# Performance work log

Measured on AMD Instinct MI355X. Metric: run time of the kernel, lower is better.

## Reference

```python
import jax, jax.numpy as jnp
import numpy as np

B, T, V, E, H, C = 64, 512, 50257, 128, 64, 20

def _lstm_params(key, in_dim, scale=0.05):
    k1, k2, k3 = jax.random.split(key, 3)
    return (jax.random.normal(k1, (in_dim, 4 * H)) * scale,
            jax.random.normal(k2, (H, 4 * H)) * scale,
            jax.random.normal(k3, (4 * H,)) * scale)

def setup_inputs():
    key = jax.random.key(0)
    ks = jax.random.split(key, 10)
    lengths = jax.random.randint(ks[0], (B,), T // 4, T + 1)
    mask = (jnp.arange(T)[None, :] < lengths[:, None]).astype(jnp.int32)
    ids = jax.random.randint(ks[1], (B, T), 1, V) * mask  # pad id 0 past length
    positions = jnp.broadcast_to(jnp.arange(T, dtype=jnp.int32), (B, T))
    x = jnp.stack([ids, positions, mask], axis=1)  # [B,3,T]
    inp = {"x": x,
           "word_emb": jax.random.normal(ks[2], (V, E)) * 0.05,
           "pos_emb": jax.random.normal(ks[3], (V, E)) * 0.05}
    for name, in_dim, kk in [("f0", E, ks[4]), ("f1", H, ks[5]), ("b0", E, ks[6]), ("b1", H, ks[7])]:
        Wx, Wh, b = _lstm_params(kk, in_dim)
        inp["wx_" + name] = Wx
        inp["wh_" + name] = Wh
        inp["b_" + name] = b
    inp["dense_w"] = jax.random.normal(ks[8], (H, C)) * 0.05
    inp["dense_b"] = jnp.zeros((C,), jnp.float32)
    return inp

def _lstm_layer(xs, mask, Wx, Wh, b, backwards):
    # xs: [B,T,D], mask: [B,T] bool. Keras masking semantics: at masked steps
    # hidden/cell state (and emitted output) carry over from the previous step.
    # go_backwards reverses inputs AND mask, and does NOT re-reverse outputs
    # (that is the raw keras LSTM behaviour without the Bidirectional wrapper).
    if backwards:
        xs = xs[:, ::-1]
        mask = mask[:, ::-1]
    xT = jnp.swapaxes(xs, 0, 1)    # [T,B,D]
    mT = jnp.swapaxes(mask, 0, 1)  # [T,B]
    h0 = jnp.zeros((xs.shape[0], H), xs.dtype)
    c0 = h0
    def step(carry, inp):
        h, c = carry
        x_t, m_t = inp
        z = x_t @ Wx + h @ Wh + b  # [B,4H], keras gate order i,f,g,o
        i = jax.nn.sigmoid(z[:, :H])
        f = jax.nn.sigmoid(z[:, H:2 * H])
        g = jnp.tanh(z[:, 2 * H:3 * H])
        o = jax.nn.sigmoid(z[:, 3 * H:])
        c_new = f * c + i * g
        h_new = o * jnp.tanh(c_new)
        m = m_t[:, None]
        h2 = jnp.where(m, h_new, h)
        c2 = jnp.where(m, c_new, c)
        return (h2, c2), h2
    _, hs = jax.lax.scan(step, (h0, c0), (xT, mT))
    return jnp.swapaxes(hs, 0, 1)  # [B,T,H]

def reference(x, word_emb, pos_emb, wx_f0, wh_f0, b_f0, wx_f1, wh_f1, b_f1,
              wx_b0, wh_b0, b_b0, wx_b1, wh_b1, b_b1, dense_w, dense_b):
    ids, positions, attn = x[:, 0, :], x[:, 1, :], x[:, 2, :]
    mask = attn.astype(bool)
    emb = word_emb[ids] + pos_emb[positions]  # [B,T,E]
    f = _lstm_layer(emb, mask, wx_f0, wh_f0, b_f0, False)
    f = _lstm_layer(f, mask, wx_f1, wh_f1, b_f1, False)
    bo = _lstm_layer(emb, mask, wx_b0, wh_b0, b_b0, True)
    bo = _lstm_layer(bo, mask, wx_b1, wh_b1, b_b1, True)
    # Concatenate(axis=1) stacks [fwd_out, bwd_out] along TIME, dense+softmax
    # per step, then [:, -1, :] -> only the last step of the backward stack
    # reaches the output (faithful to the original module).
    last = bo[:, -1, :]
    return jax.nn.softmax(last @ dense_w + dense_b, axis=-1)  # [B,C]
```

## Files before the change

### kernel.cpp

```cpp
#include <hip/hip_runtime.h>
#include <hip/hip_bf16.h>

#define Bn 64
#define Tn 512
#define En 128
#define Hn 64
#define Gn 256
#define Cn 20

__device__ __forceinline__ float sigf(float x)      { return 1.f/(1.f+__expf(-x)); }
__device__ __forceinline__ float tanhfast(float x)  { return 2.f/(1.f+__expf(-2.f*x)) - 1.f; }

__global__ __launch_bounds__(256, 1) void emb_proj_kernel(
    const int* __restrict__ x, const float* __restrict__ word_emb,
    const float* __restrict__ pos_emb, const float* __restrict__ wx,
    const float* __restrict__ bias, float* __restrict__ z0)
{
  __shared__ float emb[64][En];
  __shared__ float wxl[32][Gn];
  const int tid  = threadIdx.x;
  const int row0 = blockIdx.x * 64;

  #pragma unroll
  for (int it = 0; it < 8; ++it) {
    int idx = it*256 + tid;
    int rr  = idx >> 5;
    int e4  = (idx & 31) << 2;
    int r   = row0 + rr;
    int b   = r >> 9;
    int t   = r & (Tn-1);
    int id  = x[b*3*Tn + t];
    float4 we = *reinterpret_cast<const float4*>(&word_emb[(size_t)id*En + e4]);
    float4 pe = *reinterpret_cast<const float4*>(&pos_emb[(size_t)t*En + e4]);
    *reinterpret_cast<float4*>(&emb[rr][e4]) =
        make_float4(we.x+pe.x, we.y+pe.y, we.z+pe.z, we.w+pe.w);
  }

  const int jc = tid & 63;
  const int rg = tid >> 6;
  float acc[16][4];
  float4 bb = *reinterpret_cast<const float4*>(&bias[jc*4]);
  #pragma unroll
  for (int r = 0; r < 16; ++r) { acc[r][0]=bb.x; acc[r][1]=bb.y; acc[r][2]=bb.z; acc[r][3]=bb.w; }

  for (int ec = 0; ec < 4; ++ec) {
    __syncthreads();
    #pragma unroll
    for (int it = 0; it < 8; ++it) {
      int idx = it*256 + tid;
      int ee  = idx >> 6;
      int j4  = (idx & 63) << 2;
      *reinterpret_cast<float4*>(&wxl[ee][j4]) =
          *reinterpret_cast<const float4*>(&wx[(size_t)(ec*32+ee)*Gn + j4]);
    }
    __syncthreads();
    for (int ee = 0; ee < 32; ++ee) {
      float4 w = *reinterpret_cast<const float4*>(&wxl[ee][jc*4]);
      #pragma unroll
      for (int r = 0; r < 16; ++r) {
        float xv = emb[rg*16+r][ec*32+ee];
        acc[r][0] = fmaf(xv, w.x, acc[r][0]);
        acc[r][1] = fmaf(xv, w.y, acc[r][1]);
        acc[r][2] = fmaf(xv, w.z, acc[r][2]);
        acc[r][3] = fmaf(xv, w.w, acc[r][3]);
      }
    }
  }
  #pragma unroll
  for (int r = 0; r < 16; ++r) {
    size_t row = (size_t)row0 + rg*16 + r;
    *reinterpret_cast<float4*>(&z0[row*Gn + jc*4]) =
        make_float4(acc[r][0], acc[r][1], acc[r][2], acc[r][3]);
  }
}

__global__ __launch_bounds__(256, 1) void zx1_gemm_kernel(
    const float* __restrict__ hb0, const float* __restrict__ wx,
    const float* __restrict__ bias, float* __restrict__ zx1)
{
  __shared__ float xl[64][Hn];
  __shared__ float wl[32][Gn];
  const int tid  = threadIdx.x;
  const int row0 = blockIdx.x * 64;

  #pragma unroll
  for (int it = 0; it < 4; ++it) {
    int idx = it*256 + tid;
    int rr  = idx >> 4;
    int e4  = (idx & 15) << 2;
    *reinterpret_cast<float4*>(&xl[rr][e4]) =
        *reinterpret_cast<const float4*>(&hb0[((size_t)row0+rr)*Hn + e4]);
  }

  const int jc = tid & 63;
  const int rg = tid >> 6;
  float acc[16][4];
  float4 bb = *reinterpret_cast<const float4*>(&bias[jc*4]);
  #pragma unroll
  for (int r = 0; r < 16; ++r) { acc[r][0]=bb.x; acc[r][1]=bb.y; acc[r][2]=bb.z; acc[r][3]=bb.w; }

  for (int kc = 0; kc < 2; ++kc) {
    __syncthreads();
    #pragma unroll
    for (int it = 0; it < 8; ++it) {
      int idx = it*256 + tid;
      int kk  = idx >> 6;
      int j4  = (idx & 63) << 2;
      *reinterpret_cast<float4*>(&wl[kk][j4]) =
          *reinterpret_cast<const float4*>(&wx[(size_t)(kc*32+kk)*Gn + j4]);
    }
    __syncthreads();
    for (int kk = 0; kk < 32; ++kk) {
      float4 w = *reinterpret_cast<const float4*>(&wl[kk][jc*4]);
      #pragma unroll
      for (int r = 0; r < 16; ++r) {
        float xv = xl[rg*16+r][kc*32+kk];
        acc[r][0] = fmaf(xv, w.x, acc[r][0]);
        acc[r][1] = fmaf(xv, w.y, acc[r][1]);
        acc[r][2] = fmaf(xv, w.z, acc[r][2]);
        acc[r][3] = fmaf(xv, w.w, acc[r][3]);
      }
    }
  }
  #pragma unroll
  for (int r = 0; r < 16; ++r) {
    size_t row = (size_t)row0 + rg*16 + r;
    *reinterpret_cast<float4*>(&zx1[row*Gn + jc*4]) =
        make_float4(acc[r][0], acc[r][1], acc[r][2], acc[r][3]);
  }
}

#define WAVE_BARRIER()                                        \
  do {                                                        \
    asm volatile("s_waitcnt lgkmcnt(0)" ::: "memory");        \
    __builtin_amdgcn_sched_barrier(0);                        \
    __builtin_amdgcn_s_barrier();                             \
    __builtin_amdgcn_sched_barrier(0);                        \
  } while (0)

#define PLOAD(dst, t_)                                                      \
  { const float* pp_ = zr + (size_t)(t_)*Gn + tid;                          \
    asm volatile("global_load_dword %0, %1, off" : "=v"(dst) : "v"(pp_)); }

template<bool IS_B0>
__global__ __launch_bounds__(256, 1) void lstm_fast(
    const int* __restrict__ x, const float* __restrict__ z,
    const float* __restrict__ wh, float* __restrict__ hb0,
    const float* __restrict__ dw, const float* __restrict__ db,
    float* __restrict__ out)
{
  const int b   = blockIdx.x;
  const int tid = threadIdx.x;
  const int wv  = tid >> 6;
  const int l   = tid & 63;

  __shared__ __align__(16) float z_s[2][Gn];
  __shared__ __align__(16) float h_own[4][Hn];
  __shared__ float sm[2][32];
  __shared__ int slen;

  if (tid == 0) slen = 0;
  __syncthreads();
  {
    int m0 = x[b*3*Tn + 2*Tn + tid];
    int m1 = x[b*3*Tn + 2*Tn + 256 + tid];
    atomicAdd(&slen, m0 + m1);
  }
  float wcol[Hn];
  #pragma unroll
  for (int k = 0; k < Hn; ++k) wcol[k] = wh[(size_t)k*Gn + tid];
  h_own[wv][l] = 0.f;
  __syncthreads();
  const int len = slen;

  const float* zr   = z   + (size_t)b*Tn*Gn;
  float*       hout = hb0 + (size_t)b*Tn*Hn;
  float c = 0.f, h = 0.f;

  if (IS_B0) {
    for (int r = len + (tid >> 4); r < Tn; r += 16)
      *reinterpret_cast<float4*>(&hout[(size_t)r*Hn + (tid & 15)*4]) =
          make_float4(0.f, 0.f, 0.f, 0.f);
  }

  float zp0, zp1, zp2, zp3;
  PLOAD(zp0, IS_B0 ? len-1 : Tn-len);
  PLOAD(zp1, IS_B0 ? len-2 : Tn-len+1);
  PLOAD(zp2, IS_B0 ? len-3 : Tn-len+2);
  PLOAD(zp3, IS_B0 ? len-4 : Tn-len+3);
  asm volatile("s_waitcnt vmcnt(0)" ::: "memory");
  __builtin_amdgcn_sched_barrier(0);

#define STEP(s_, ZREG)                                                       \
  {                                                                          \
    if (IS_B0) asm volatile("s_waitcnt vmcnt(7)" ::: "memory");              \
    else       asm volatile("s_waitcnt vmcnt(3)" ::: "memory");              \
    __builtin_amdgcn_sched_barrier(0);                                       \
    float a0 = ZREG, a1 = 0.f, a2 = 0.f, a3 = 0.f;                           \
    _Pragma("unroll")                                                        \
    for (int k4 = 0; k4 < 16; ++k4) {                                        \
      float4 hv = *reinterpret_cast<const float4*>(&h_own[wv][k4*4]);        \
      a0 = fmaf(hv.x, wcol[k4*4+0], a0);                                     \
      a1 = fmaf(hv.y, wcol[k4*4+1], a1);                                     \
      a2 = fmaf(hv.z, wcol[k4*4+2], a2);                                     \
      a3 = fmaf(hv.w, wcol[k4*4+3], a3);                                     \
    }                                                                        \
    {                        \
      int tn_ = IS_B0 ? (len-5-(s_)) : (Tn-len+(s_)+4);                      \
      tn_ = tn_ < 0 ? 0 : (tn_ > Tn-1 ? Tn-1 : tn_);                         \
      const float* pp_ = zr + (size_t)tn_*Gn + tid;                          \
      asm volatile("global_load_dword %0, %1, off" : "=v"(ZREG) : "v"(pp_)); \
    }                                                                        \
    z_s[(s_)&1][tid] = (a0+a1)+(a2+a3);                                      \
    WAVE_BARRIER();                                                          \
    float g0 = z_s[(s_)&1][l],      g1 = z_s[(s_)&1][Hn+l];                  \
    float g2 = z_s[(s_)&1][2*Hn+l], g3 = z_s[(s_)&1][3*Hn+l];                \
    float ig = sigf(g0), fg = sigf(g1);                                      \
    float gg = tanhfast(g2), og = sigf(g3);                                  \
    float cn_ = fmaf(fg, c, ig*gg);                                          \
    float hn_ = og * tanhfast(cn_);                                          \
    bool act_ = (s_) < len;                                                  \
    c = act_ ? cn_ : c;                                                      \
    h = act_ ? hn_ : h;                                                      \
    h_own[wv][l] = h;                                                        \
    if (IS_B0) {                                                             \
      int ts_ = len-1-(s_); ts_ = ts_ < 0 ? 0 : ts_;                         \
      float* sp_ = hout + (size_t)ts_*Hn + l;                                \
      asm volatile("global_store_dword %0, %1, off" :: "v"(sp_), "v"(h));    \
    }                                                                        \
  }

  const int lenr = (len + 3) & ~3;
  for (int s = 0; s < lenr; s += 4) {
    STEP(s+0, zp0);
    STEP(s+1, zp1);
    STEP(s+2, zp2);
    STEP(s+3, zp3);
  }
#undef STEP

  asm volatile("s_waitcnt vmcnt(0)" ::: "memory");
  __builtin_amdgcn_sched_barrier(0);

  if (!IS_B0) {
    if (tid < Cn) {
      float lg = db[tid];
      #pragma unroll
      for (int k = 0; k < Hn; ++k) lg = fmaf(h_own[0][k], dw[k*Cn + tid], lg);
      sm[0][tid] = lg;
    }
    if (tid < Cn) {
      float m = sm[0][0];
      #pragma unroll
      for (int k = 1; k < Cn; ++k) m = fmaxf(m, sm[0][k]);
      float e = __expf(sm[0][tid] - m);
      sm[1][tid] = e;
      float ssum = 0.f;
      #pragma unroll
      for (int k = 0; k < Cn; ++k) ssum += sm[1][k];
      out[b*Cn + tid] = e / ssum;
    }
  }
}

extern "C" void kernel_launch(void* const* d_in, const int* in_sizes, int n_in,
                              void* d_out, int out_size, void* d_ws, size_t ws_size,
                              hipStream_t stream)
{
  const int*   x        = (const int*)  d_in[0];
  const float* word_emb = (const float*)d_in[1];
  const float* pos_emb  = (const float*)d_in[2];
  const float* wx_b0    = (const float*)d_in[9];
  const float* wh_b0    = (const float*)d_in[10];
  const float* b_b0     = (const float*)d_in[11];
  const float* wx_b1    = (const float*)d_in[12];
  const float* wh_b1    = (const float*)d_in[13];
  const float* b_b1     = (const float*)d_in[14];
  const float* dw       = (const float*)d_in[15];
  const float* db       = (const float*)d_in[16];
  float* out = (float*)d_out;

  float* z0  = (float*)d_ws;
  float* hb0 = z0 + (size_t)Bn*Tn*Gn;

  emb_proj_kernel<<<dim3((Bn*Tn)/64), dim3(256), 0, stream>>>(
      x, word_emb, pos_emb, wx_b0, b_b0, z0);
  lstm_fast<true><<<dim3(Bn), dim3(256), 0, stream>>>(
      x, z0, wh_b0, hb0, nullptr, nullptr, nullptr);
  zx1_gemm_kernel<<<dim3((Bn*Tn)/64), dim3(256), 0, stream>>>(
      hb0, wx_b1, b_b1, z0);
  lstm_fast<false><<<dim3(Bn), dim3(256), 0, stream>>>(
      x, z0, wh_b1, hb0, dw, db, out);
}
```

Measured before the change: 646.2 us.

## Run each LSTM recurrence in a single wavefront with packed FMA gates

Replaces the 4-wave per-sequence LSTM block with one 64-lane wave where each lane computes all four gates for its hidden unit using v_pk_fma_f32 and register-resident weights. This removes the per-step workgroup barrier and the LDS exchange of gate pre-activations. In exchange, each lane does four times the dot-product work and four activations per step, with higher register pressure; z prefetch is restructured to two steps ahead with four loads each.

```diff
diff --git a/kernel.cpp b/kernel.cpp
--- a/kernel.cpp
+++ b/kernel.cpp
@@ -7,6 +7,8 @@
 #define Hn 64
 #define Gn 256
 #define Cn 20
+
+typedef float f32x2 __attribute__((ext_vector_type(2)));
 
 __device__ __forceinline__ float sigf(float x)      { return 1.f/(1.f+__expf(-x)); }
 __device__ __forceinline__ float tanhfast(float x)  { return 2.f/(1.f+__expf(-2.f*x)) - 1.f; }
@@ -130,135 +132,140 @@
   }
 }
 
-#define WAVE_BARRIER()                                        \
-  do {                                                        \
-    asm volatile("s_waitcnt lgkmcnt(0)" ::: "memory");        \
-    __builtin_amdgcn_sched_barrier(0);                        \
-    __builtin_amdgcn_s_barrier();                             \
-    __builtin_amdgcn_sched_barrier(0);                        \
-  } while (0)
-
-#define PLOAD(dst, t_)                                                      \
-  { const float* pp_ = zr + (size_t)(t_)*Gn + tid;                          \
-    asm volatile("global_load_dword %0, %1, off" : "=v"(dst) : "v"(pp_)); }
+#define PK_FMA(acc, hp, wp) \
+  asm("v_pk_fma_f32 %0, %1, %2, %0" : "+v"(acc) : "v"(hp), "v"(wp))
 
 template<bool IS_B0>
-__global__ __launch_bounds__(256, 1) void lstm_fast(
+__global__ __launch_bounds__(64, 1) void lstm_wave(
     const int* __restrict__ x, const float* __restrict__ z,
     const float* __restrict__ wh, float* __restrict__ hb0,
     const float* __restrict__ dw, const float* __restrict__ db,
     float* __restrict__ out)
 {
-  const int b   = blockIdx.x;
-  const int tid = threadIdx.x;
-  const int wv  = tid >> 6;
-  const int l   = tid & 63;
-
-  __shared__ __align__(16) float z_s[2][Gn];
-  __shared__ __align__(16) float h_own[4][Hn];
-  __shared__ float sm[2][32];
-  __shared__ int slen;
-
-  if (tid == 0) slen = 0;
-  __syncthreads();
-  {
-    int m0 = x[b*3*Tn + 2*Tn + tid];
-    int m1 = x[b*3*Tn + 2*Tn + 256 + tid];
-    atomicAdd(&slen, m0 + m1);
-  }
-  float wcol[Hn];
-  #pragma unroll
-  for (int k = 0; k < Hn; ++k) wcol[k] = wh[(size_t)k*Gn + tid];
-  h_own[wv][l] = 0.f;
-  __syncthreads();
-  const int len = slen;
-
+  const int b = blockIdx.x;
+  const int l = threadIdx.x;
+  __shared__ __align__(16) float h_lds[Hn];
+  __shared__ float sm0[32], sm1[32];
+
+  int msum = 0;
+  #pragma unroll
+  for (int i = 0; i < 8; ++i) msum += x[b*3*Tn + 2*Tn + i*64 + l];
+  #pragma unroll
+  for (int off = 1; off < 64; off <<= 1) msum += __shfl_xor(msum, off, 64);
+  const int len = msum;
+
+  f32x2 wi[32], wf[32], wg[32], wo[32];
+  #pragma unroll
+  for (int k2 = 0; k2 < 32; ++k2) {
+    const float* r0 = wh + (size_t)(2*k2)*Gn;
+    const float* r1 = wh + (size_t)(2*k2+1)*Gn;
+    wi[k2] = f32x2{r0[l],       r1[l]};
+    wf[k2] = f32x2{r0[64+l],    r1[64+l]};
+    wg[k2] = f32x2{r0[128+l],   r1[128+l]};
+    wo[k2] = f32x2{r0[192+l],   r1[192+l]};
+  }
+
+  h_lds[l] = 0.f;
+  float c = 0.f, h = 0.f;
   const float* zr   = z   + (size_t)b*Tn*Gn;
   float*       hout = hb0 + (size_t)b*Tn*Hn;
-  float c = 0.f, h = 0.f;
 
   if (IS_B0) {
-    for (int r = len + (tid >> 4); r < Tn; r += 16)
-      *reinterpret_cast<float4*>(&hout[(size_t)r*Hn + (tid & 15)*4]) =
+    for (int r = len + (l >> 4); r < Tn; r += 4)
+      *reinterpret_cast<float4*>(&hout[(size_t)r*Hn + (l & 15)*4]) =
           make_float4(0.f, 0.f, 0.f, 0.f);
   }
 
-  float zp0, zp1, zp2, zp3;
-  PLOAD(zp0, IS_B0 ? len-1 : Tn-len);
-  PLOAD(zp1, IS_B0 ? len-2 : Tn-len+1);
-  PLOAD(zp2, IS_B0 ? len-3 : Tn-len+2);
-  PLOAD(zp3, IS_B0 ? len-4 : Tn-len+3);
+  float za0, za1, za2, za3, zb0, zb1, zb2, zb3;
+  {
+    const float* p = zr + (size_t)(IS_B0 ? len-1 : Tn-len)*Gn + l;
+    asm volatile("global_load_dword %0, %1, off"            : "=v"(za0) : "v"(p));
+    asm volatile("global_load_dword %0, %1, off offset:256" : "=v"(za1) : "v"(p));
+    asm volatile("global_load_dword %0, %1, off offset:512" : "=v"(za2) : "v"(p));
+    asm volatile("global_load_dword %0, %1, off offset:768" : "=v"(za3) : "v"(p));
+  }
+  {
+    const float* p = zr + (size_t)(IS_B0 ? len-2 : Tn-len+1)*Gn + l;
+    asm volatile("global_load_dword %0, %1, off"            : "=v"(zb0) : "v"(p));
+    asm volatile("global_load_dword %0, %1, off offset:256" : "=v"(zb1) : "v"(p));
+    asm volatile("global_load_dword %0, %1, off offset:512" : "=v"(zb2) : "v"(p));
+    asm volatile("global_load_dword %0, %1, off offset:768" : "=v"(zb3) : "v"(p));
+  }
   asm volatile("s_waitcnt vmcnt(0)" ::: "memory");
   __builtin_amdgcn_sched_barrier(0);
 
-#define STEP(s_, ZREG)                                                       \
+#define STEP(s_, Z0, Z1, Z2, Z3)                                             \
   {                                                                          \
-    if (IS_B0) asm volatile("s_waitcnt vmcnt(7)" ::: "memory");              \
-    else       asm volatile("s_waitcnt vmcnt(3)" ::: "memory");              \
+    if (IS_B0) asm volatile("s_waitcnt vmcnt(5)" ::: "memory");              \
+    else       asm volatile("s_waitcnt vmcnt(4)" ::: "memory");              \
     __builtin_amdgcn_sched_barrier(0);                                       \
-    float a0 = ZREG, a1 = 0.f, a2 = 0.f, a3 = 0.f;                           \
+    f32x2 ai = {0.f,0.f}, af2 = {0.f,0.f}, ag2 = {0.f,0.f}, ao2 = {0.f,0.f}; \
     _Pragma("unroll")                                                        \
     for (int k4 = 0; k4 < 16; ++k4) {                                        \
-      float4 hv = *reinterpret_cast<const float4*>(&h_own[wv][k4*4]);        \
-      a0 = fmaf(hv.x, wcol[k4*4+0], a0);                                     \
-      a1 = fmaf(hv.y, wcol[k4*4+1], a1);                                     \
-      a2 = fmaf(hv.z, wcol[k4*4+2], a2);                                     \
-      a3 = fmaf(hv.w, wcol[k4*4+3], a3);                                     \
+      float4 hv = *reinterpret_cast<const float4*>(&h_lds[k4*4]);            \
+      f32x2 h01 = {hv.x, hv.y}, h23 = {hv.z, hv.w};                          \
+      PK_FMA(ai,  h01, wi[2*k4]);  PK_FMA(ai,  h23, wi[2*k4+1]);             \
+      PK_FMA(af2, h01, wf[2*k4]);  PK_FMA(af2, h23, wf[2*k4+1]);             \
+      PK_FMA(ag2, h01, wg[2*k4]);  PK_FMA(ag2, h23, wg[2*k4+1]);             \
+      PK_FMA(ao2, h01, wo[2*k4]);  PK_FMA(ao2, h23, wo[2*k4+1]);             \
     }                                                                        \
-    {                        \
-      int tn_ = IS_B0 ? (len-5-(s_)) : (Tn-len+(s_)+4);                      \
-      tn_ = tn_ < 0 ? 0 : (tn_ > Tn-1 ? Tn-1 : tn_);                         \
-      const float* pp_ = zr + (size_t)tn_*Gn + tid;                          \
-      asm volatile("global_load_dword %0, %1, off" : "=v"(ZREG) : "v"(pp_)); \
-    }                                                                        \
-    z_s[(s_)&1][tid] = (a0+a1)+(a2+a3);                                      \
-    WAVE_BARRIER();                                                          \
-    float g0 = z_s[(s_)&1][l],      g1 = z_s[(s_)&1][Hn+l];                  \
-    float g2 = z_s[(s_)&1][2*Hn+l], g3 = z_s[(s_)&1][3*Hn+l];                \
-    float ig = sigf(g0), fg = sigf(g1);                                      \
-    float gg = tanhfast(g2), og = sigf(g3);                                  \
+    float a_i = (ai[0]+ai[1])   + (Z0);                                      \
+    float a_f = (af2[0]+af2[1]) + (Z1);                                      \
+    float a_g = (ag2[0]+ag2[1]) + (Z2);                                      \
+    float a_o = (ao2[0]+ao2[1]) + (Z3);                                      \
+    float ig = sigf(a_i), fg = sigf(a_f);                                    \
+    float gg = tanhfast(a_g), og = sigf(a_o);                                \
     float cn_ = fmaf(fg, c, ig*gg);                                          \
     float hn_ = og * tanhfast(cn_);                                          \
     bool act_ = (s_) < len;                                                  \
     c = act_ ? cn_ : c;                                                      \
     h = act_ ? hn_ : h;                                                      \
-    h_own[wv][l] = h;                                                        \
+    h_lds[l] = h;                                                            \
     if (IS_B0) {                                                             \
       int ts_ = len-1-(s_); ts_ = ts_ < 0 ? 0 : ts_;                         \
       float* sp_ = hout + (size_t)ts_*Hn + l;                                \
       asm volatile("global_store_dword %0, %1, off" :: "v"(sp_), "v"(h));    \
     }                                                                        \
-  }
-
-  const int lenr = (len + 3) & ~3;
-  for (int s = 0; s < lenr; s += 4) {
-    STEP(s+0, zp0);
-    STEP(s+1, zp1);
-    STEP(s+2, zp2);
-    STEP(s+3, zp3);
+    {                                                                        \
+      int tn_ = IS_B0 ? (len-3-(s_)) : (Tn-len+(s_)+2);                      \
+      tn_ = tn_ < 0 ? 0 : (tn_ > Tn-1 ? Tn-1 : tn_);                         \
+      const float* p_ = zr + (size_t)tn_*Gn + l;                             \
+      asm volatile("global_load_dword %0, %1, off"            : "=v"(Z0) : "v"(p_)); \
+      asm volatile("global_load_dword %0, %1, off offset:256" : "=v"(Z1) : "v"(p_)); \
+      asm volatile("global_load_dword %0, %1, off offset:512" : "=v"(Z2) : "v"(p_)); \
+      asm volatile("global_load_dword %0, %1, off offset:768" : "=v"(Z3) : "v"(p_)); \
+    }                                                                        \
+  }
+
+  const int lenr = (len + 1) & ~1;
+  for (int s = 0; s < lenr; s += 2) {
+    STEP(s+0, za0, za1, za2, za3);
+    STEP(s+1, zb0, zb1, zb2, zb3);
   }
 #undef STEP
 
   asm volatile("s_waitcnt vmcnt(0)" ::: "memory");
+  asm volatile("" :: "v"(za0), "v"(za1), "v"(za2), "v"(za3),
+                     "v"(zb0), "v"(zb1), "v"(zb2), "v"(zb3));
   __builtin_amdgcn_sched_barrier(0);
 
   if (!IS_B0) {
-    if (tid < Cn) {
-      float lg = db[tid];
-      #pragma unroll
-      for (int k = 0; k < Hn; ++k) lg = fmaf(h_own[0][k], dw[k*Cn + tid], lg);
-      sm[0][tid] = lg;
-    }
-    if (tid < Cn) {
-      float m = sm[0][0];
-      #pragma unroll
-      for (int k = 1; k < Cn; ++k) m = fmaxf(m, sm[0][k]);
-      float e = __expf(sm[0][tid] - m);
-      sm[1][tid] = e;
+    if (l < Cn) {
+      float lg = db[l];
+      #pragma unroll
+      for (int k = 0; k < Hn; ++k) lg = fmaf(h_lds[k], dw[k*Cn + l], lg);
+      sm0[l] = lg;
+    }
+    if (l < Cn) {
+      float m = sm0[0];
+      #pragma unroll
+      for (int k = 1; k < Cn; ++k) m = fmaxf(m, sm0[k]);
+      float e = __expf(sm0[l] - m);
+      sm1[l] = e;
       float ssum = 0.f;
       #pragma unroll
-      for (int k = 0; k < Cn; ++k) ssum += sm[1][k];
-      out[b*Cn + tid] = e / ssum;
+      for (int k = 0; k < Cn; ++k) ssum += sm1[k];
+      out[b*Cn + l] = e / ssum;
     }
   }
 }
@@ -285,10 +292,10 @@
 
   emb_proj_kernel<<<dim3((Bn*Tn)/64), dim3(256), 0, stream>>>(
       x, word_emb, pos_emb, wx_b0, b_b0, z0);
-  lstm_fast<true><<<dim3(Bn), dim3(256), 0, stream>>>(
+  lstm_wave<true><<<dim3(Bn), dim3(64), 0, stream>>>(
       x, z0, wh_b0, hb0, nullptr, nullptr, nullptr);
   zx1_gemm_kernel<<<dim3((Bn*Tn)/64), dim3(256), 0, stream>>>(
       hb0, wx_b1, b_b1, z0);
-  lstm_fast<false><<<dim3(Bn), dim3(256), 0, stream>>>(
+  lstm_wave<false><<<dim3(Bn), dim3(64), 0, stream>>>(
       x, z0, wh_b1, hb0, dw, db, out);
 }
```

Result: slower. 1.275 ms (+97.4%).
